# Kernel optimization log

Measured on AMD Instinct MI355X. Metric: run time of the kernel, lower is better.

## Reference

```python
import jax, jax.numpy as jnp
import numpy as np

N_NODES = 10000
N_EDGES = 250000
FEAT = 128
HEADS = 4
N_RBF = 50
CUTOFF = 5.0
EPS = 1e-15
LN_EPS = 1e-5


def setup_inputs() -> dict:
    key = jax.random.key(0)
    ks = jax.random.split(key, 12)
    F, HF = FEAT, HEADS * FEAT

    def lin(k, fi, fo):
        return (jax.random.normal(k, (fi, fo), jnp.float32) / np.sqrt(fi)).astype(jnp.float32)

    return {
        "s_j": jax.random.normal(ks[0], (N_NODES, F), jnp.float32),
        "v_j": jax.random.normal(ks[1], (N_NODES, F, 3), jnp.float32),
        "r_ij": jax.random.normal(ks[2], (N_EDGES, 3), jnp.float32) * 2.0,
        "nbrs": jax.random.randint(ks[3], (N_EDGES, 2), 0, N_NODES, dtype=jnp.int64) if jax.config.read('jax_enable_x64') else jax.random.randint(ks[3], (N_EDGES, 2), 0, N_NODES),
        "ln_gamma": jnp.ones((F,), jnp.float32),
        "ln_beta": jnp.zeros((F,), jnp.float32),
        "Wq": lin(ks[4], F, HF), "bq": jnp.zeros((HF,), jnp.float32),
        "Wk": lin(ks[5], F, HF), "bk": jnp.zeros((HF,), jnp.float32),
        "Wv": lin(ks[6], F, HF), "bv": jnp.zeros((HF,), jnp.float32),
        "Wdk": lin(ks[7], N_RBF, HF), "bdk": jnp.zeros((HF,), jnp.float32),
        "Wdv": lin(ks[8], N_RBF, HF), "bdv": jnp.zeros((HF,), jnp.float32),
        "Wd": lin(ks[9], HF, 3 * F), "bd": jnp.zeros((3 * F,), jnp.float32),
    }


def _forward(s_j, v_j, r_ij, nbrs, ln_gamma, ln_beta,
             Wq, bq, Wk, bk, Wv, bv, Wdk, bdk, Wdv, bdv, Wd, bd):
    E, F, H = r_ij.shape[0], s_j.shape[-1], HEADS
    # preprocess_r: dist and unit vectors
    dist = jnp.sqrt((r_ij ** 2 + EPS).sum(-1))          # [E]
    unit = r_ij / dist[:, None]                          # [E, 3]

    # LayerNorm (biased variance, like torch)
    mu = s_j.mean(-1, keepdims=True)
    var = s_j.var(-1, keepdims=True)
    x = (s_j - mu) / jnp.sqrt(var + LN_EPS) * ln_gamma + ln_beta  # [N, F]

    # node projections per head (head dim == feat_dim, TorchMD-Net style)
    q = (x @ Wq + bq).reshape(-1, H, F)
    k = (x @ Wk + bk).reshape(-1, H, F)
    v = (x @ Wv + bv).reshape(-1, H, F)

    # Gaussian RBF expansion of distances
    mus = jnp.linspace(0.0, CUTOFF, N_RBF, dtype=dist.dtype)
    width = mus[1] - mus[0]
    gamma = 0.5 / (width * width)
    rbf = jnp.exp(-gamma * (dist[:, None] - mus) ** 2)   # [E, n_rbf]

    dk = jax.nn.silu(rbf @ Wdk + bdk).reshape(E, H, F)   # distance filters
    dv = jax.nn.silu(rbf @ Wdv + bdv).reshape(E, H, F)

    i_dst = nbrs[:, 0]
    j_src = nbrs[:, 1]

    # attention over edges: silu(sum_f q_i * k_j * dk)
    attn = jax.nn.silu((q[i_dst] * k[j_src] * dk).sum(-1))  # [E, H]
    msg = (v[j_src] * dv * attn[:, :, None]).reshape(E, H * F)  # [E, H*F]

    out = (msg @ Wd + bd).reshape(E, 3, F)               # inv_out
    split0 = out[:, 0, :][:, :, None]                    # [E, F, 1]
    split1 = out[:, 1, :]                                # [E, F]
    split2 = out[:, 2, :][:, :, None]                    # [E, F, 1]

    delta_v_ij = split2 * unit[:, None, :] + split0 * v_j[j_src]  # [E, F, 3]
    delta_v_i = jax.ops.segment_sum(delta_v_ij, i_dst, num_segments=s_j.shape[0])
    delta_s_i = jax.ops.segment_sum(split1, i_dst, num_segments=s_j.shape[0])
    return delta_s_i, delta_v_i


def reference(s_j, v_j, r_ij, nbrs, ln_gamma, ln_beta,
              Wq, bq, Wk, bk, Wv, bv, Wdk, bdk, Wdv, bdv, Wd, bd):
    return _forward(s_j, v_j, r_ij, nbrs, ln_gamma, ln_beta,
                    Wq, bq, Wk, bk, Wv, bv, Wdk, bdk, Wdv, bdv, Wd, bd)
```

## Files before the change

### kernel.cpp

```cpp
#include <hip/hip_runtime.h>
#include <hip/hip_bf16.h>

typedef unsigned short ushort_t;
typedef short short8 __attribute__((ext_vector_type(8)));
typedef short short4v __attribute__((ext_vector_type(4)));
typedef float floatx4 __attribute__((ext_vector_type(4)));

#define FEAT 128
#define HF   512
#define NRBF 50
#define NNODE 10000
#define NEDGE 250000
#define NCHUNK 3907

__device__ __forceinline__ float b2f(unsigned int b){
    unsigned int u = (b & 0xffffu) << 16;
    float f; __builtin_memcpy(&f, &u, 4); return f;
}
__device__ __forceinline__ unsigned short f2b(float f){
    __hip_bfloat16 h = __float2bfloat16(f);
    unsigned short u; __builtin_memcpy(&u, &h, 2); return u;
}
__device__ __forceinline__ float silu_f(float x){ return x / (1.f + __expf(-x)); }

__device__ __forceinline__ bool is_fp32(const void* lng){
    return ((((const unsigned int*)lng)[0]) & 0xffffu) == 0u;
}
__device__ __forceinline__ float ld_f(const void* p, long idx, bool fp32){
    return fp32 ? ((const float*)p)[idx] : b2f(((const ushort_t*)p)[idx]);
}
__device__ __forceinline__ ushort_t ld_bf(const void* p, long idx, bool fp32){
    return fp32 ? f2b(((const float*)p)[idx]) : ((const ushort_t*)p)[idx];
}

__global__ __launch_bounds__(256) void k_sentinel(float* __restrict__ out){
    int x = blockIdx.x*256 + threadIdx.x;
    if (x < NNODE*FEAT*4) out[x] = 1.0f;
}

__global__ __launch_bounds__(256) void k_nbrs(const unsigned int* __restrict__ raw, int* __restrict__ out){
    int x = blockIdx.x*256 + threadIdx.x;
    if (x >= 2*NEDGE) return;
    unsigned int m = raw[1]|raw[3]|raw[5]|raw[7]|raw[9]|raw[11]|raw[13]|raw[15];
    int v = (m == 0u) ? (int)raw[2*x] : (int)raw[x];
    out[x] = ((unsigned)v < (unsigned)NNODE) ? v : 0;
}

__global__ __launch_bounds__(256) void k_count(const int* __restrict__ nb32, int* __restrict__ cnt){
    int x = blockIdx.x*256 + threadIdx.x;
    if (x >= NEDGE) return;
    atomicAdd(&cnt[nb32[2*x]], 1);
}
__global__ __launch_bounds__(256) void k_scan(const int* __restrict__ cnt, int* __restrict__ cursor){
    __shared__ int part[256];
    __shared__ int base[256];
    const int t = threadIdx.x;
    const int start = t*40;
    int s = 0;
    for (int u=0; u<40; u++){ int idx = start+u; if (idx < NNODE) s += cnt[idx]; }
    part[t] = s;
    __syncthreads();
    if (t == 0){
        int run = 0;
        for (int u=0; u<256; u++){ base[u] = run; run += part[u]; }
    }
    __syncthreads();
    int run = base[t];
    for (int u=0; u<40; u++){
        int idx = start+u;
        if (idx < NNODE){ cursor[idx] = run; run += cnt[idx]; }
    }
}
__global__ __launch_bounds__(256) void k_place(const int* __restrict__ nb32,
                                               int* __restrict__ cursor, int* __restrict__ perm){
    int x = blockIdx.x*256 + threadIdx.x;
    if (x >= NEDGE) return;
    int i = nb32[2*x];
    int pos = atomicAdd(&cursor[i], 1);
    perm[pos] = x;
}

__global__ __launch_bounds__(256) void k_conv(
    const void* ln_g, const void* ln_b, const void* bq, const void* bk, const void* bv,
    const void* bdk, const void* bdv, const void* bd, ushort_t* __restrict__ cb)
{
    const int t = threadIdx.x;
    const bool fp32 = is_fp32(ln_g);
    const void* srcs[8] = {ln_g, ln_b, bq, bk, bv, bdk, bdv, bd};
    const int offs[9] = {0,128,256,768,1280,1792,2304,2816,3200};
    for (int s=0; s<8; s++){
        int cnt = offs[s+1]-offs[s];
        for (int x=t; x<cnt; x+=256) cb[offs[s]+x] = ld_bf(srcs[s], x, fp32);
    }
}

__global__ __launch_bounds__(256) void k_vconv(const void* __restrict__ v_j,
                                               const void* __restrict__ lng,
                                               ushort_t* __restrict__ vjb){
    int x = blockIdx.x*256 + threadIdx.x;
    if (x >= NNODE*FEAT*3) return;
    vjb[x] = ld_bf(v_j, x, is_fp32(lng));
}

__global__ __launch_bounds__(256) void k_prep(
    const void* __restrict__ Wq, const void* __restrict__ Wk, const void* __restrict__ Wv,
    const void* __restrict__ Wdk, const void* __restrict__ Wdv, const void* __restrict__ Wd,
    const void* __restrict__ lng,
    ushort_t* __restrict__ WqT, ushort_t* __restrict__ WkT, ushort_t* __restrict__ WvT,
    ushort_t* __restrict__ WdkT, ushort_t* __restrict__ WdvT, ushort_t* __restrict__ WdT)
{
    const bool fp32 = is_fp32(lng);
    int idx = blockIdx.x*256 + threadIdx.x;
    if (idx < 3*65536){
        int mat = idx >> 16; int o = idx & 65535;
        int c = o >> 7, r = o & 127;
        const void* src = (mat==0)?Wq:((mat==1)?Wk:Wv);
        ushort_t* dst = (mat==0)?WqT:((mat==1)?WkT:WvT);
        dst[o] = ld_bf(src, r*HF + c, fp32);
    } else if (idx < 3*65536 + 2*32768){
        int o2 = idx - 3*65536; int mat = o2 >> 15; int o = o2 & 32767;
        int c = o >> 6, kk = o & 63;
        const void* src = mat ? Wdv : Wdk;
        ushort_t* dst = mat ? WdvT : WdkT;
        dst[o] = (kk < NRBF) ? ld_bf(src, kk*HF + c, fp32) : (ushort_t)0;
    } else {
        int o = idx - (3*65536 + 2*32768);
        int c = o >> 9, kk = o & 511;
        WdT[o] = ld_bf(Wd, kk*384 + c, fp32);
    }
}

__global__ __launch_bounds__(256) void k_qkv2(
    const void* __restrict__ s_j, const void* __restrict__ lng, const ushort_t* __restrict__ cb,
    const ushort_t* __restrict__ WqT, const ushort_t* __restrict__ WkT, const ushort_t* __restrict__ WvT,
    ushort_t* __restrict__ q, ushort_t* __restrict__ k, ushort_t* __restrict__ v)
{
    __shared__ __align__(16) ushort_t xlds[16][136];
    const int t = threadIdx.x;
    const int n = t >> 4, g = t & 15;
    const long node = (long)blockIdx.x*16 + n;
    const bool fp32 = is_fp32(lng);

    float xs[8];
    if (fp32){
        const float* sf = (const float*)s_j + node*FEAT + g*8;
        #pragma unroll
        for (int i=0;i<8;i++) xs[i] = sf[i];
    } else {
        short8 sv = *reinterpret_cast<const short8*>((const ushort_t*)s_j + node*FEAT + g*8);
        #pragma unroll
        for (int i=0;i<8;i++) xs[i] = b2f((unsigned short)sv[i]);
    }
    float sum = 0.f, ss = 0.f;
    #pragma unroll
    for (int i=0;i<8;i++){ sum += xs[i]; ss += xs[i]*xs[i]; }
    #pragma unroll
    for (int off=8; off; off>>=1){ sum += __shfl_xor(sum, off, 16); ss += __shfl_xor(ss, off, 16); }
    float mu = sum * (1.f/FEAT);
    float var = ss * (1.f/FEAT) - mu*mu;
    float sc = rsqrtf(var + 1e-5f);
    short8 gv  = *reinterpret_cast<const short8*>(cb + g*8);
    short8 bv2 = *reinterpret_cast<const short8*>(cb + 128 + g*8);
    short8 xv;
    #pragma unroll
    for (int i=0;i<8;i++){
        float val = (xs[i]-mu)*sc*b2f((unsigned short)gv[i]) + b2f((unsigned short)bv2[i]);
        xv[i] = (short)f2b(val);
    }
    *reinterpret_cast<short8*>(&xlds[n][g*8]) = xv;
    __syncthreads();

    const int lane = t & 63, w = t >> 6;
    const int col = lane & 15, quad = lane >> 4;
    short8 a[4];
    #pragma unroll
    for (int ks=0; ks<4; ks++)
        a[ks] = *reinterpret_cast<const short8*>(&xlds[col][ks*32 + quad*8]);

    for (int ii=0; ii<24; ii++){
        int nt = w + ii*4;
        int mat = nt >> 5, o0 = (nt & 31) << 4;
        const ushort_t* WT  = (mat==0)?WqT:((mat==1)?WkT:WvT);
        const ushort_t* bia = cb + 256 + mat*512;
        ushort_t* outp      = (mat==0)?q:((mat==1)?k:v);
        floatx4 acc = {0.f,0.f,0.f,0.f};
        #pragma unroll
        for (int ks=0; ks<4; ks++){
            short8 b = *reinterpret_cast<const short8*>(WT + (o0+col)*FEAT + ks*32 + quad*8);
            acc = __builtin_amdgcn_mfma_f32_16x16x32_bf16(a[ks], b, acc, 0, 0, 0);
        }
        float bc = b2f(bia[o0+col]);
        #pragma unroll
        for (int reg=0; reg<4; reg++){
            int row = quad*4 + reg;
            outp[((long)blockIdx.x*16 + row)*HF + o0 + col] = f2b(acc[reg] + bc);
        }
    }
}

struct __align__(16) EdgeSmem {
    int   i[64];
    int   jv[64];
    float unit[64][3];
    ushort_t rbf[4][16][72];
    union {
        ushort_t dkv[4][16][520];
        float    outb[32*385];
    };
};

__global__ __launch_bounds__(256, 2) void k_edge(
    const void* __restrict__ r_ij, const void* __restrict__ lng,
    const int* __restrict__ nbrs32, const int* __restrict__ perm,
    const ushort_t* __restrict__ q, const ushort_t* __restrict__ k, const ushort_t* __restrict__ v,
    const ushort_t* __restrict__ vjb,
    const ushort_t* __restrict__ WdkT, const ushort_t* __restrict__ WdvT,
    const ushort_t* __restrict__ cb,
    const ushort_t* __restrict__ WdT,
    float* __restrict__ acc_s, float* __restrict__ acc_v)
{
    __shared__ EdgeSmem sm;
    const int t = threadIdx.x;
    const long chunk = (long)(blockIdx.x & 7) * 489 + (blockIdx.x >> 3);
    if (chunk >= NCHUNK) return;
    const long e0 = chunk * 64;
    const int nvalid = (NEDGE - e0 < 64) ? (int)(NEDGE - e0) : 64;
    const bool fp32 = is_fp32(lng);
    const int lane = t & 63, w = t >> 6;
    const int col = lane & 15, quad = lane >> 4;
    const int eA = t >> 4, g = t & 15;
    const int h = g >> 2, sub = g & 3;

    short8 qf[4][4], kf[4][4];
    int jA_s[4];

    #pragma unroll
    for (int s=0; s<4; s++){
        const long eidx = e0 + s*16 + eA;
        const long ep = perm[(eidx < NEDGE) ? eidx : (NEDGE-1)];
        const int iA = nbrs32[2*ep];
        const int jA = nbrs32[2*ep+1];
        jA_s[s] = jA;
        float rx = ld_f(r_ij, ep*3+0, fp32);
        float ry = ld_f(r_ij, ep*3+1, fp32);
        float rz = ld_f(r_ij, ep*3+2, fp32);
        float d = sqrtf(rx*rx + ry*ry + rz*rz + 3e-15f);
        float inv = 1.f/d;
        if (g == 0){
            sm.i[s*16+eA] = iA; sm.jv[s*16+eA] = jA;
            sm.unit[s*16+eA][0] = rx*inv; sm.unit[s*16+eA][1] = ry*inv; sm.unit[s*16+eA][2] = rz*inv;
        }
        const float WIDTH = 5.f/49.f;
        const float GAMMA = 0.5f/(WIDTH*WIDTH);
        short4v rv;
        #pragma unroll
        for (int u=0; u<4; u++){
            int m = g*4 + u;
            float val = 0.f;
            if (m < NRBF){ float dm = d - (float)m*WIDTH; val = __expf(-GAMMA*dm*dm); }
            rv[u] = (short)f2b(val);
        }
        *reinterpret_cast<short4v*>(&sm.rbf[s][eA][g*4]) = rv;
        const ushort_t* qp = q + (long)iA*HF + h*128 + sub*32;
        const ushort_t* kp = k + (long)jA*HF + h*128 + sub*32;
        #pragma unroll
        for (int r=0; r<4; r++){
            qf[s][r] = *reinterpret_cast<const short8*>(qp + r*8);
            kf[s][r] = *reinterpret_cast<const short8*>(kp + r*8);
        }
    }
    __syncthreads();

    {
        for (int ii=0; ii<8; ii++){
            int nt = w + ii*4;
            int o0 = nt << 4;
            short8 b0 = *reinterpret_cast<const short8*>(WdkT + (o0+col)*64 + quad*8);
            short8 b1 = *reinterpret_cast<const short8*>(WdkT + (o0+col)*64 + 32 + quad*8);
            float bc = b2f(cb[1792 + o0 + col]);
            #pragma unroll
            for (int s=0; s<4; s++){
                short8 a0 = *reinterpret_cast<const short8*>(&sm.rbf[s][col][quad*8]);
                short8 a1 = *reinterpret_cast<const short8*>(&sm.rbf[s][col][32 + quad*8]);
                floatx4 ac = {0.f,0.f,0.f,0.f};
                ac = __builtin_amdgcn_mfma_f32_16x16x32_bf16(a0, b0, ac, 0, 0, 0);
                ac = __builtin_amdgcn_mfma_f32_16x16x32_bf16(a1, b1, ac, 0, 0, 0);
                #pragma unroll
                for (int reg=0; reg<4; reg++){
                    int row = quad*4 + reg;
                    sm.dkv[s][row][o0+col] = f2b(silu_f(ac[reg] + bc));
                }
            }
        }
    }
    __syncthreads();

    float at[4];
    short8 vf[4][4];
    {
        #pragma unroll
        for (int s=0; s<4; s++){
            const ushort_t* vp = v + (long)jA_s[s]*HF + g*32;
            #pragma unroll
            for (int r=0; r<4; r++) vf[s][r] = *reinterpret_cast<const short8*>(vp + r*8);
        }
        #pragma unroll
        for (int s=0; s<4; s++){
            const ushort_t* dkp = &sm.dkv[s][eA][h*128 + sub*32];
            float p = 0.f;
            #pragma unroll
            for (int r=0; r<4; r++){
                short8 d8 = *reinterpret_cast<const short8*>(dkp + r*8);
                #pragma unroll
                for (int u=0; u<8; u++)
                    p += b2f((unsigned short)qf[s][r][u]) * b2f((unsigned short)kf[s][r][u]) * b2f((unsigned short)d8[u]);
            }
            p += __shfl_xor(p, 1);
            p += __shfl_xor(p, 2);
            at[s] = silu_f(p);
        }
    }
    __syncthreads();

    {
        for (int ii=0; ii<8; ii++){
            int nt = w + ii*4;
            int o0 = nt << 4;
            short8 b0 = *reinterpret_cast<const short8*>(WdvT + (o0+col)*64 + quad*8);
            short8 b1 = *reinterpret_cast<const short8*>(WdvT + (o0+col)*64 + 32 + quad*8);
            float bc = b2f(cb[2304 + o0 + col]);
            #pragma unroll
            for (int s=0; s<4; s++){
                short8 a0 = *reinterpret_cast<const short8*>(&sm.rbf[s][col][quad*8]);
                short8 a1 = *reinterpret_cast<const short8*>(&sm.rbf[s][col][32 + quad*8]);
                floatx4 ac = {0.f,0.f,0.f,0.f};
                ac = __builtin_amdgcn_mfma_f32_16x16x32_bf16(a0, b0, ac, 0, 0, 0);
                ac = __builtin_amdgcn_mfma_f32_16x16x32_bf16(a1, b1, ac, 0, 0, 0);
                #pragma unroll
                for (int reg=0; reg<4; reg++){
                    int row = quad*4 + reg;
                    sm.dkv[s][row][o0+col] = f2b(silu_f(ac[reg] + bc));
                }
            }
        }
    }
    __syncthreads();

    #pragma unroll
    for (int s=0; s<4; s++){
        ushort_t* dvp = &sm.dkv[s][eA][g*32];
        #pragma unroll
        for (int r=0; r<4; r++){
            short8 d8 = *reinterpret_cast<const short8*>(dvp + r*8);
            short8 o8;
            #pragma unroll
            for (int u=0; u<8; u++)
                o8[u] = (short)f2b(b2f((unsigned short)vf[s][r][u]) * b2f((unsigned short)d8[u]) * at[s]);
            *reinterpret_cast<short8*>(dvp + r*8) = o8;
        }
    }
    __syncthreads();

    floatx4 acc[4][6];
    {
        #pragma unroll
        for (int s=0; s<4; s++)
            #pragma unroll
            for (int ii=0; ii<6; ii++) acc[s][ii] = (floatx4){0.f,0.f,0.f,0.f};
        for (int ks=0; ks<16; ks++){
            short8 a0 = *reinterpret_cast<const short8*>(&sm.dkv[0][col][ks*32 + quad*8]);
            short8 a1 = *reinterpret_cast<const short8*>(&sm.dkv[1][col][ks*32 + quad*8]);
            short8 a2 = *reinterpret_cast<const short8*>(&sm.dkv[2][col][ks*32 + quad*8]);
            short8 a3 = *reinterpret_cast<const short8*>(&sm.dkv[3][col][ks*32 + quad*8]);
            #pragma unroll
            for (int ii=0; ii<6; ii++){
                int o0 = (w + ii*4) << 4;
                short8 b = *reinterpret_cast<const short8*>(WdT + (o0+col)*HF + ks*32 + quad*8);
                acc[0][ii] = __builtin_amdgcn_mfma_f32_16x16x32_bf16(a0, b, acc[0][ii], 0, 0, 0);
                acc[1][ii] = __builtin_amdgcn_mfma_f32_16x16x32_bf16(a1, b, acc[1][ii], 0, 0, 0);
                acc[2][ii] = __builtin_amdgcn_mfma_f32_16x16x32_bf16(a2, b, acc[2][ii], 0, 0, 0);
                acc[3][ii] = __builtin_amdgcn_mfma_f32_16x16x32_bf16(a3, b, acc[3][ii], 0, 0, 0);
            }
        }
    }
    __syncthreads();

    {
        const int f = t & 127, half = t >> 7;
        int   cur_i = -1;
        float as = 0.f, av0 = 0.f, av1 = 0.f, av2 = 0.f;
        #pragma unroll
        for (int p=0; p<2; p++){
            #pragma unroll
            for (int ii=0; ii<6; ii++){
                int o0 = (w + ii*4) << 4;
                float bc = b2f(cb[2816 + o0 + col]);
                #pragma unroll
                for (int sl=0; sl<2; sl++){
                    int s = 2*p + sl;
                    #pragma unroll
                    for (int reg=0; reg<4; reg++){
                        int lrow = sl*16 + quad*4 + reg;
                        sm.outb[lrow*385 + o0 + col] = acc[s][ii][reg] + bc;
                    }
                }
            }
            __syncthreads();

            float vjx[16][3];
            #pragma unroll
            for (int u=0; u<16; u++){
                int e = p*32 + half*16 + u;
                const ushort_t* vp = vjb + (long)sm.jv[e]*384 + 3*f;
                vjx[u][0] = b2f(vp[0]); vjx[u][1] = b2f(vp[1]); vjx[u][2] = b2f(vp[2]);
            }
            #pragma unroll
            for (int u=0; u<16; u++){
                int el = half*16 + u;
                int e  = p*32 + el;
                if (e < nvalid){
                    int ie = sm.i[e];
                    if (ie != cur_i){
                        if (cur_i >= 0){
                            atomicAdd(&acc_s[(long)cur_i*FEAT + f], as);
                            float* ap = acc_v + ((long)cur_i*FEAT + f)*3;
                            atomicAdd(ap+0, av0); atomicAdd(ap+1, av1); atomicAdd(ap+2, av2);
                        }
                        cur_i = ie; as = 0.f; av0 = 0.f; av1 = 0.f; av2 = 0.f;
                    }
                    float o0v = sm.outb[el*385 + f];
                    float o1v = sm.outb[el*385 + 128 + f];
                    float o2v = sm.outb[el*385 + 256 + f];
                    as  += o1v;
                    av0 += o2v*sm.unit[e][0] + o0v*vjx[u][0];
                    av1 += o2v*sm.unit[e][1] + o0v*vjx[u][1];
                    av2 += o2v*sm.unit[e][2] + o0v*vjx[u][2];
                }
            }
            __syncthreads();
        }
        if (cur_i >= 0){
            atomicAdd(&acc_s[(long)cur_i*FEAT + f], as);
            float* ap = acc_v + ((long)cur_i*FEAT + f)*3;
            atomicAdd(ap+0, av0); atomicAdd(ap+1, av1); atomicAdd(ap+2, av2);
        }
    }
}

extern "C" void kernel_launch(void* const* d_in, const int* in_sizes, int n_in,
                              void* d_out, int out_size, void* d_ws, size_t ws_size,
                              hipStream_t stream)
{
    const void* s_j  = d_in[0];
    const void* v_j  = d_in[1];
    const void* r_ij = d_in[2];
    const unsigned int* nbrs_raw = (const unsigned int*)d_in[3];
    const void* ln_g = d_in[4];
    const void* ln_b = d_in[5];
    const void* Wq = d_in[6];   const void* bq  = d_in[7];
    const void* Wk = d_in[8];   const void* bk  = d_in[9];
    const void* Wv = d_in[10];  const void* bv  = d_in[11];
    const void* Wdk= d_in[12];  const void* bdk = d_in[13];
    const void* Wdv= d_in[14];  const void* bdv = d_in[15];
    const void* Wd = d_in[16];  const void* bd  = d_in[17];

    const size_t NEED = 43883904;
    if (ws_size < NEED){
        k_sentinel<<<20000, 256, 0, stream>>>((float*)d_out);
        return;
    }

    char* ws = (char*)d_ws;
    ushort_t* q    = (ushort_t*)(ws);
    ushort_t* vjb  = (ushort_t*)(ws + 10240000);
    int*      perm = (int*)(ws + 17920000);
    int*      cnt  = (int*)(ws + 18920000);
    int*      curs = (int*)(ws + 18960000);
    ushort_t* kk   = (ushort_t*)(ws + 20480000);
    ushort_t* vv   = (ushort_t*)(ws + 30720000);
    ushort_t* WqT  = (ushort_t*)(ws + 40960000);
    ushort_t* WkT  = (ushort_t*)(ws + 41091072);
    ushort_t* WvT  = (ushort_t*)(ws + 41222144);
    ushort_t* WdkT = (ushort_t*)(ws + 41353216);
    ushort_t* WdvT = (ushort_t*)(ws + 41418752);
    ushort_t* WdT  = (ushort_t*)(ws + 41484288);
    int*      nb32 = (int*)(ws + 41877504);
    ushort_t* cb   = (ushort_t*)(ws + 43877504);

    float* acc_s = (float*)d_out;
    float* acc_v = acc_s + 1280000;

    hipMemsetAsync(d_out, 0, 20480000, stream);
    hipMemsetAsync(cnt, 0, NNODE*sizeof(int), stream);
    k_nbrs <<<1954, 256, 0, stream>>>(nbrs_raw, nb32);
    k_count<<<977, 256, 0, stream>>>(nb32, cnt);
    k_scan <<<1, 256, 0, stream>>>(cnt, curs);
    k_place<<<977, 256, 0, stream>>>(nb32, curs, perm);
    k_conv <<<1, 256, 0, stream>>>(ln_g, ln_b, bq, bk, bv, bdk, bdv, bd, cb);
    k_vconv<<<15000, 256, 0, stream>>>(v_j, ln_g, vjb);
    k_prep <<<1792, 256, 0, stream>>>(Wq,Wk,Wv,Wdk,Wdv,Wd, ln_g, WqT,WkT,WvT,WdkT,WdvT,WdT);
    k_qkv2 <<<625, 256, 0, stream>>>(s_j, ln_g, cb, WqT, WkT, WvT, q, kk, vv);
    k_edge <<<3912, 256, 0, stream>>>(r_ij, ln_g, nb32, perm, q, kk, vv, vjb,
                                      WdkT, WdvT, cb, WdT,
                                      acc_s, acc_v);
}
```

Before: 690.4 us.

## Double edge tile to 128 edges per block with 512 threads

The edge kernel now processes 128 edges per block with 8 waves instead of 64 edges with 4 waves. Each Wd/Wdk/Wdv B-fragment loaded from global memory feeds 8 MFMA row tiles instead of 4, which halves weight traffic per edge. Per-thread accumulator state is rebalanced (acc[8][3]) and the scatter phase runs in four passes of 32 edges. Shared memory per block roughly doubles, so fewer blocks fit per CU. The larger chunks also add more synchronisation within each block.

```diff
diff --git a/kernel.cpp b/kernel.cpp
--- a/kernel.cpp
+++ b/kernel.cpp
@@ -11,7 +11,7 @@
 #define NRBF 50
 #define NNODE 10000
 #define NEDGE 250000
-#define NCHUNK 3907
+#define NCHUNK 1954
 
 __device__ __forceinline__ float b2f(unsigned int b){
     unsigned int u = (b & 0xffffu) << 16;
@@ -199,17 +199,17 @@
 }
 
 struct __align__(16) EdgeSmem {
-    int   i[64];
-    int   jv[64];
-    float unit[64][3];
-    ushort_t rbf[4][16][72];
+    int   i[128];
+    int   jv[128];
+    float unit[128][3];
+    ushort_t rbf[128][72];
     union {
-        ushort_t dkv[4][16][520];
+        ushort_t dkv[128][520];
         float    outb[32*385];
     };
 };
 
-__global__ __launch_bounds__(256, 2) void k_edge(
+__global__ __launch_bounds__(512, 2) void k_edge(
     const void* __restrict__ r_ij, const void* __restrict__ lng,
     const int* __restrict__ nbrs32, const int* __restrict__ perm,
     const ushort_t* __restrict__ q, const ushort_t* __restrict__ k, const ushort_t* __restrict__ v,
@@ -221,10 +221,10 @@
 {
     __shared__ EdgeSmem sm;
     const int t = threadIdx.x;
-    const long chunk = (long)(blockIdx.x & 7) * 489 + (blockIdx.x >> 3);
+    const long chunk = (long)(blockIdx.x & 7) * 245 + (blockIdx.x >> 3);
     if (chunk >= NCHUNK) return;
-    const long e0 = chunk * 64;
-    const int nvalid = (NEDGE - e0 < 64) ? (int)(NEDGE - e0) : 64;
+    const long e0 = chunk * 128;
+    const int nvalid = (NEDGE - e0 < 128) ? (int)(NEDGE - e0) : 128;
     const bool fp32 = is_fp32(lng);
     const int lane = t & 63, w = t >> 6;
     const int col = lane & 15, quad = lane >> 4;
@@ -236,7 +236,8 @@
 
     #pragma unroll
     for (int s=0; s<4; s++){
-        const long eidx = e0 + s*16 + eA;
+        const int e_loc = s*32 + eA;
+        const long eidx = e0 + e_loc;
         const long ep = perm[(eidx < NEDGE) ? eidx : (NEDGE-1)];
         const int iA = nbrs32[2*ep];
         const int jA = nbrs32[2*ep+1];
@@ -247,8 +248,8 @@
         float d = sqrtf(rx*rx + ry*ry + rz*rz + 3e-15f);
         float inv = 1.f/d;
         if (g == 0){
-            sm.i[s*16+eA] = iA; sm.jv[s*16+eA] = jA;
-            sm.unit[s*16+eA][0] = rx*inv; sm.unit[s*16+eA][1] = ry*inv; sm.unit[s*16+eA][2] = rz*inv;
+            sm.i[e_loc] = iA; sm.jv[e_loc] = jA;
+            sm.unit[e_loc][0] = rx*inv; sm.unit[e_loc][1] = ry*inv; sm.unit[e_loc][2] = rz*inv;
         }
         const float WIDTH = 5.f/49.f;
         const float GAMMA = 0.5f/(WIDTH*WIDTH);
@@ -260,7 +261,7 @@
             if (m < NRBF){ float dm = d - (float)m*WIDTH; val = __expf(-GAMMA*dm*dm); }
             rv[u] = (short)f2b(val);
         }
-        *reinterpret_cast<short4v*>(&sm.rbf[s][eA][g*4]) = rv;
+        *reinterpret_cast<short4v*>(&sm.rbf[e_loc][g*4]) = rv;
         const ushort_t* qp = q + (long)iA*HF + h*128 + sub*32;
         const ushort_t* kp = k + (long)jA*HF + h*128 + sub*32;
         #pragma unroll
@@ -272,23 +273,23 @@
     __syncthreads();
 
     {
-        for (int ii=0; ii<8; ii++){
-            int nt = w + ii*4;
+        for (int ii=0; ii<4; ii++){
+            int nt = w + ii*8;
             int o0 = nt << 4;
             short8 b0 = *reinterpret_cast<const short8*>(WdkT + (o0+col)*64 + quad*8);
             short8 b1 = *reinterpret_cast<const short8*>(WdkT + (o0+col)*64 + 32 + quad*8);
             float bc = b2f(cb[1792 + o0 + col]);
             #pragma unroll
-            for (int s=0; s<4; s++){
-                short8 a0 = *reinterpret_cast<const short8*>(&sm.rbf[s][col][quad*8]);
-                short8 a1 = *reinterpret_cast<const short8*>(&sm.rbf[s][col][32 + quad*8]);
+            for (int st=0; st<8; st++){
+                short8 a0 = *reinterpret_cast<const short8*>(&sm.rbf[st*16+col][quad*8]);
+                short8 a1 = *reinterpret_cast<const short8*>(&sm.rbf[st*16+col][32 + quad*8]);
                 floatx4 ac = {0.f,0.f,0.f,0.f};
                 ac = __builtin_amdgcn_mfma_f32_16x16x32_bf16(a0, b0, ac, 0, 0, 0);
                 ac = __builtin_amdgcn_mfma_f32_16x16x32_bf16(a1, b1, ac, 0, 0, 0);
                 #pragma unroll
                 for (int reg=0; reg<4; reg++){
-                    int row = quad*4 + reg;
-                    sm.dkv[s][row][o0+col] = f2b(silu_f(ac[reg] + bc));
+                    int row = st*16 + quad*4 + reg;
+                    sm.dkv[row][o0+col] = f2b(silu_f(ac[reg] + bc));
                 }
             }
         }
@@ -306,7 +307,8 @@
         }
         #pragma unroll
         for (int s=0; s<4; s++){
-            const ushort_t* dkp = &sm.dkv[s][eA][h*128 + sub*32];
+            const int e_loc = s*32 + eA;
+            const ushort_t* dkp = &sm.dkv[e_loc][h*128 + sub*32];
             float p = 0.f;
             #pragma unroll
             for (int r=0; r<4; r++){
@@ -323,23 +325,23 @@
     __syncthreads();
 
     {
-        for (int ii=0; ii<8; ii++){
-            int nt = w + ii*4;
+        for (int ii=0; ii<4; ii++){
+            int nt = w + ii*8;
             int o0 = nt << 4;
             short8 b0 = *reinterpret_cast<const short8*>(WdvT + (o0+col)*64 + quad*8);
             short8 b1 = *reinterpret_cast<const short8*>(WdvT + (o0+col)*64 + 32 + quad*8);
             float bc = b2f(cb[2304 + o0 + col]);
             #pragma unroll
-            for (int s=0; s<4; s++){
-                short8 a0 = *reinterpret_cast<const short8*>(&sm.rbf[s][col][quad*8]);
-                short8 a1 = *reinterpret_cast<const short8*>(&sm.rbf[s][col][32 + quad*8]);
+            for (int st=0; st<8; st++){
+                short8 a0 = *reinterpret_cast<const short8*>(&sm.rbf[st*16+col][quad*8]);
+                short8 a1 = *reinterpret_cast<const short8*>(&sm.rbf[st*16+col][32 + quad*8]);
                 floatx4 ac = {0.f,0.f,0.f,0.f};
                 ac = __builtin_amdgcn_mfma_f32_16x16x32_bf16(a0, b0, ac, 0, 0, 0);
                 ac = __builtin_amdgcn_mfma_f32_16x16x32_bf16(a1, b1, ac, 0, 0, 0);
                 #pragma unroll
                 for (int reg=0; reg<4; reg++){
-                    int row = quad*4 + reg;
-                    sm.dkv[s][row][o0+col] = f2b(silu_f(ac[reg] + bc));
+                    int row = st*16 + quad*4 + reg;
+                    sm.dkv[row][o0+col] = f2b(silu_f(ac[reg] + bc));
                 }
             }
         }
@@ -348,7 +350,8 @@
 
     #pragma unroll
     for (int s=0; s<4; s++){
-        ushort_t* dvp = &sm.dkv[s][eA][g*32];
+        const int e_loc = s*32 + eA;
+        ushort_t* dvp = &sm.dkv[e_loc][g*32];
         #pragma unroll
         for (int r=0; r<4; r++){
             short8 d8 = *reinterpret_cast<const short8*>(dvp + r*8);
@@ -361,62 +364,61 @@
     }
     __syncthreads();
 
-    floatx4 acc[4][6];
+    floatx4 acc[8][3];
     {
         #pragma unroll
-        for (int s=0; s<4; s++)
-            #pragma unroll
-            for (int ii=0; ii<6; ii++) acc[s][ii] = (floatx4){0.f,0.f,0.f,0.f};
+        for (int st=0; st<8; st++)
+            #pragma unroll
+            for (int ii=0; ii<3; ii++) acc[st][ii] = (floatx4){0.f,0.f,0.f,0.f};
         for (int ks=0; ks<16; ks++){
-            short8 a0 = *reinterpret_cast<const short8*>(&sm.dkv[0][col][ks*32 + quad*8]);
-            short8 a1 = *reinterpret_cast<const short8*>(&sm.dkv[1][col][ks*32 + quad*8]);
-            short8 a2 = *reinterpret_cast<const short8*>(&sm.dkv[2][col][ks*32 + quad*8]);
-            short8 a3 = *reinterpret_cast<const short8*>(&sm.dkv[3][col][ks*32 + quad*8]);
-            #pragma unroll
-            for (int ii=0; ii<6; ii++){
-                int o0 = (w + ii*4) << 4;
+            short8 a[8];
+            #pragma unroll
+            for (int st=0; st<8; st++)
+                a[st] = *reinterpret_cast<const short8*>(&sm.dkv[st*16+col][ks*32 + quad*8]);
+            #pragma unroll
+            for (int ii=0; ii<3; ii++){
+                int o0 = (w + ii*8) << 4;
                 short8 b = *reinterpret_cast<const short8*>(WdT + (o0+col)*HF + ks*32 + quad*8);
-                acc[0][ii] = __builtin_amdgcn_mfma_f32_16x16x32_bf16(a0, b, acc[0][ii], 0, 0, 0);
-                acc[1][ii] = __builtin_amdgcn_mfma_f32_16x16x32_bf16(a1, b, acc[1][ii], 0, 0, 0);
-                acc[2][ii] = __builtin_amdgcn_mfma_f32_16x16x32_bf16(a2, b, acc[2][ii], 0, 0, 0);
-                acc[3][ii] = __builtin_amdgcn_mfma_f32_16x16x32_bf16(a3, b, acc[3][ii], 0, 0, 0);
+                #pragma unroll
+                for (int st=0; st<8; st++)
+                    acc[st][ii] = __builtin_amdgcn_mfma_f32_16x16x32_bf16(a[st], b, acc[st][ii], 0, 0, 0);
             }
         }
     }
     __syncthreads();
 
     {
-        const int f = t & 127, half = t >> 7;
+        const int f = t & 127, grp = t >> 7;
         int   cur_i = -1;
         float as = 0.f, av0 = 0.f, av1 = 0.f, av2 = 0.f;
         #pragma unroll
-        for (int p=0; p<2; p++){
-            #pragma unroll
-            for (int ii=0; ii<6; ii++){
-                int o0 = (w + ii*4) << 4;
+        for (int p=0; p<4; p++){
+            #pragma unroll
+            for (int ii=0; ii<3; ii++){
+                int o0 = (w + ii*8) << 4;
                 float bc = b2f(cb[2816 + o0 + col]);
                 #pragma unroll
                 for (int sl=0; sl<2; sl++){
-                    int s = 2*p + sl;
+                    int st = 2*p + sl;
                     #pragma unroll
                     for (int reg=0; reg<4; reg++){
                         int lrow = sl*16 + quad*4 + reg;
-                        sm.outb[lrow*385 + o0 + col] = acc[s][ii][reg] + bc;
+                        sm.outb[lrow*385 + o0 + col] = acc[st][ii][reg] + bc;
                     }
                 }
             }
             __syncthreads();
 
-            float vjx[16][3];
-            #pragma unroll
-            for (int u=0; u<16; u++){
-                int e = p*32 + half*16 + u;
+            float vjx[8][3];
+            #pragma unroll
+            for (int u=0; u<8; u++){
+                int e = p*32 + grp*8 + u;
                 const ushort_t* vp = vjb + (long)sm.jv[e]*384 + 3*f;
                 vjx[u][0] = b2f(vp[0]); vjx[u][1] = b2f(vp[1]); vjx[u][2] = b2f(vp[2]);
             }
             #pragma unroll
-            for (int u=0; u<16; u++){
-                int el = half*16 + u;
+            for (int u=0; u<8; u++){
+                int el = grp*8 + u;
                 int e  = p*32 + el;
                 if (e < nvalid){
                     int ie = sm.i[e];
@@ -500,7 +502,7 @@
     k_vconv<<<15000, 256, 0, stream>>>(v_j, ln_g, vjb);
     k_prep <<<1792, 256, 0, stream>>>(Wq,Wk,Wv,Wdk,Wdv,Wd, ln_g, WqT,WkT,WvT,WdkT,WdvT,WdT);
     k_qkv2 <<<625, 256, 0, stream>>>(s_j, ln_g, cb, WqT, WkT, WvT, q, kk, vv);
-    k_edge <<<3912, 256, 0, stream>>>(r_ij, ln_g, nb32, perm, q, kk, vv, vjb,
+    k_edge <<<1960, 512, 0, stream>>>(r_ij, ln_g, nb32, perm, q, kk, vv, vjb,
                                       WdkT, WdvT, cb, WdT,
                                       acc_s, acc_v);
 }
```

Result: slower. 738.4 us (+7.0%).

## Fuse small preprocessing kernels and process two node tiles per QKV block

Applied to the files above, without the earlier changes.

Folds the neighbor-count atomic pass and the v_j bf16 conversion into the k_nbrs kernel, and moves the bias/LayerNorm parameter conversion into an extra block of k_prep, removing three separate launches. The QKV projection kernel now handles 32 nodes per block, reusing each loaded weight fragment for two MFMA tiles and halving the grid. This cuts launch overhead and weight reloads, at the cost of a grid-stride conversion loop inside k_nbrs and a clamped, guarded tail for the last node tile.

```diff
diff --git a/kernel.cpp b/kernel.cpp
--- a/kernel.cpp
+++ b/kernel.cpp
@@ -38,19 +38,23 @@
     if (x < NNODE*FEAT*4) out[x] = 1.0f;
 }
 
-__global__ __launch_bounds__(256) void k_nbrs(const unsigned int* __restrict__ raw, int* __restrict__ out){
+__global__ __launch_bounds__(256) void k_nbrs(const unsigned int* __restrict__ raw,
+                                              int* __restrict__ out, int* __restrict__ cnt,
+                                              const void* __restrict__ v_j,
+                                              const void* __restrict__ lng,
+                                              ushort_t* __restrict__ vjb){
     int x = blockIdx.x*256 + threadIdx.x;
+    const bool fp32 = is_fp32(lng);
+    for (long y = x; y < (long)NNODE*FEAT*3; y += 500224)
+        vjb[y] = ld_bf(v_j, y, fp32);
     if (x >= 2*NEDGE) return;
     unsigned int m = raw[1]|raw[3]|raw[5]|raw[7]|raw[9]|raw[11]|raw[13]|raw[15];
     int v = (m == 0u) ? (int)raw[2*x] : (int)raw[x];
-    out[x] = ((unsigned)v < (unsigned)NNODE) ? v : 0;
-}
-
-__global__ __launch_bounds__(256) void k_count(const int* __restrict__ nb32, int* __restrict__ cnt){
-    int x = blockIdx.x*256 + threadIdx.x;
-    if (x >= NEDGE) return;
-    atomicAdd(&cnt[nb32[2*x]], 1);
-}
+    v = ((unsigned)v < (unsigned)NNODE) ? v : 0;
+    out[x] = v;
+    if (!(x & 1)) atomicAdd(&cnt[v], 1);
+}
+
 __global__ __launch_bounds__(256) void k_scan(const int* __restrict__ cnt, int* __restrict__ cursor){
     __shared__ int part[256];
     __shared__ int base[256];
@@ -80,36 +84,27 @@
     perm[pos] = x;
 }
 
-__global__ __launch_bounds__(256) void k_conv(
-    const void* ln_g, const void* ln_b, const void* bq, const void* bk, const void* bv,
-    const void* bdk, const void* bdv, const void* bd, ushort_t* __restrict__ cb)
-{
-    const int t = threadIdx.x;
-    const bool fp32 = is_fp32(ln_g);
-    const void* srcs[8] = {ln_g, ln_b, bq, bk, bv, bdk, bdv, bd};
-    const int offs[9] = {0,128,256,768,1280,1792,2304,2816,3200};
-    for (int s=0; s<8; s++){
-        int cnt = offs[s+1]-offs[s];
-        for (int x=t; x<cnt; x+=256) cb[offs[s]+x] = ld_bf(srcs[s], x, fp32);
-    }
-}
-
-__global__ __launch_bounds__(256) void k_vconv(const void* __restrict__ v_j,
-                                               const void* __restrict__ lng,
-                                               ushort_t* __restrict__ vjb){
-    int x = blockIdx.x*256 + threadIdx.x;
-    if (x >= NNODE*FEAT*3) return;
-    vjb[x] = ld_bf(v_j, x, is_fp32(lng));
-}
-
 __global__ __launch_bounds__(256) void k_prep(
     const void* __restrict__ Wq, const void* __restrict__ Wk, const void* __restrict__ Wv,
     const void* __restrict__ Wdk, const void* __restrict__ Wdv, const void* __restrict__ Wd,
-    const void* __restrict__ lng,
+    const void* __restrict__ lng, const void* __restrict__ ln_b,
+    const void* __restrict__ bq, const void* __restrict__ bk, const void* __restrict__ bv,
+    const void* __restrict__ bdk, const void* __restrict__ bdv, const void* __restrict__ bd,
     ushort_t* __restrict__ WqT, ushort_t* __restrict__ WkT, ushort_t* __restrict__ WvT,
-    ushort_t* __restrict__ WdkT, ushort_t* __restrict__ WdvT, ushort_t* __restrict__ WdT)
+    ushort_t* __restrict__ WdkT, ushort_t* __restrict__ WdvT, ushort_t* __restrict__ WdT,
+    ushort_t* __restrict__ cb)
 {
     const bool fp32 = is_fp32(lng);
+    if (blockIdx.x == 1792){
+        const int t = threadIdx.x;
+        const void* srcs[8] = {lng, ln_b, bq, bk, bv, bdk, bdv, bd};
+        const int offs[9] = {0,128,256,768,1280,1792,2304,2816,3200};
+        for (int s=0; s<8; s++){
+            int c2 = offs[s+1]-offs[s];
+            for (int x=t; x<c2; x+=256) cb[offs[s]+x] = ld_bf(srcs[s], x, fp32);
+        }
+        return;
+    }
     int idx = blockIdx.x*256 + threadIdx.x;
     if (idx < 3*65536){
         int mat = idx >> 16; int o = idx & 65535;
@@ -135,47 +130,54 @@
     const ushort_t* __restrict__ WqT, const ushort_t* __restrict__ WkT, const ushort_t* __restrict__ WvT,
     ushort_t* __restrict__ q, ushort_t* __restrict__ k, ushort_t* __restrict__ v)
 {
-    __shared__ __align__(16) ushort_t xlds[16][136];
+    __shared__ __align__(16) ushort_t xlds[2][16][136];
     const int t = threadIdx.x;
     const int n = t >> 4, g = t & 15;
-    const long node = (long)blockIdx.x*16 + n;
     const bool fp32 = is_fp32(lng);
-
-    float xs[8];
-    if (fp32){
-        const float* sf = (const float*)s_j + node*FEAT + g*8;
-        #pragma unroll
-        for (int i=0;i<8;i++) xs[i] = sf[i];
-    } else {
-        short8 sv = *reinterpret_cast<const short8*>((const ushort_t*)s_j + node*FEAT + g*8);
-        #pragma unroll
-        for (int i=0;i<8;i++) xs[i] = b2f((unsigned short)sv[i]);
-    }
-    float sum = 0.f, ss = 0.f;
+    const long base = (long)blockIdx.x*32;
+
     #pragma unroll
-    for (int i=0;i<8;i++){ sum += xs[i]; ss += xs[i]*xs[i]; }
-    #pragma unroll
-    for (int off=8; off; off>>=1){ sum += __shfl_xor(sum, off, 16); ss += __shfl_xor(ss, off, 16); }
-    float mu = sum * (1.f/FEAT);
-    float var = ss * (1.f/FEAT) - mu*mu;
-    float sc = rsqrtf(var + 1e-5f);
-    short8 gv  = *reinterpret_cast<const short8*>(cb + g*8);
-    short8 bv2 = *reinterpret_cast<const short8*>(cb + 128 + g*8);
-    short8 xv;
-    #pragma unroll
-    for (int i=0;i<8;i++){
-        float val = (xs[i]-mu)*sc*b2f((unsigned short)gv[i]) + b2f((unsigned short)bv2[i]);
-        xv[i] = (short)f2b(val);
-    }
-    *reinterpret_cast<short8*>(&xlds[n][g*8]) = xv;
+    for (int s=0; s<2; s++){
+        long node = base + s*16 + n;
+        if (node >= NNODE) node = NNODE-1;
+        float xs[8];
+        if (fp32){
+            const float* sf = (const float*)s_j + node*FEAT + g*8;
+            #pragma unroll
+            for (int i=0;i<8;i++) xs[i] = sf[i];
+        } else {
+            short8 sv = *reinterpret_cast<const short8*>((const ushort_t*)s_j + node*FEAT + g*8);
+            #pragma unroll
+            for (int i=0;i<8;i++) xs[i] = b2f((unsigned short)sv[i]);
+        }
+        float sum = 0.f, ss = 0.f;
+        #pragma unroll
+        for (int i=0;i<8;i++){ sum += xs[i]; ss += xs[i]*xs[i]; }
+        #pragma unroll
+        for (int off=8; off; off>>=1){ sum += __shfl_xor(sum, off, 16); ss += __shfl_xor(ss, off, 16); }
+        float mu = sum * (1.f/FEAT);
+        float var = ss * (1.f/FEAT) - mu*mu;
+        float sc = rsqrtf(var + 1e-5f);
+        short8 gv  = *reinterpret_cast<const short8*>(cb + g*8);
+        short8 bv2 = *reinterpret_cast<const short8*>(cb + 128 + g*8);
+        short8 xv;
+        #pragma unroll
+        for (int i=0;i<8;i++){
+            float val = (xs[i]-mu)*sc*b2f((unsigned short)gv[i]) + b2f((unsigned short)bv2[i]);
+            xv[i] = (short)f2b(val);
+        }
+        *reinterpret_cast<short8*>(&xlds[s][n][g*8]) = xv;
+    }
     __syncthreads();
 
     const int lane = t & 63, w = t >> 6;
     const int col = lane & 15, quad = lane >> 4;
-    short8 a[4];
+    short8 a0[4], a1[4];
     #pragma unroll
-    for (int ks=0; ks<4; ks++)
-        a[ks] = *reinterpret_cast<const short8*>(&xlds[col][ks*32 + quad*8]);
+    for (int ks=0; ks<4; ks++){
+        a0[ks] = *reinterpret_cast<const short8*>(&xlds[0][col][ks*32 + quad*8]);
+        a1[ks] = *reinterpret_cast<const short8*>(&xlds[1][col][ks*32 + quad*8]);
+    }
 
     for (int ii=0; ii<24; ii++){
         int nt = w + ii*4;
@@ -183,17 +185,22 @@
         const ushort_t* WT  = (mat==0)?WqT:((mat==1)?WkT:WvT);
         const ushort_t* bia = cb + 256 + mat*512;
         ushort_t* outp      = (mat==0)?q:((mat==1)?k:v);
-        floatx4 acc = {0.f,0.f,0.f,0.f};
+        floatx4 ac0 = {0.f,0.f,0.f,0.f};
+        floatx4 ac1 = {0.f,0.f,0.f,0.f};
         #pragma unroll
         for (int ks=0; ks<4; ks++){
             short8 b = *reinterpret_cast<const short8*>(WT + (o0+col)*FEAT + ks*32 + quad*8);
-            acc = __builtin_amdgcn_mfma_f32_16x16x32_bf16(a[ks], b, acc, 0, 0, 0);
+            ac0 = __builtin_amdgcn_mfma_f32_16x16x32_bf16(a0[ks], b, ac0, 0, 0, 0);
+            ac1 = __builtin_amdgcn_mfma_f32_16x16x32_bf16(a1[ks], b, ac1, 0, 0, 0);
         }
         float bc = b2f(bia[o0+col]);
         #pragma unroll
         for (int reg=0; reg<4; reg++){
             int row = quad*4 + reg;
-            outp[((long)blockIdx.x*16 + row)*HF + o0 + col] = f2b(acc[reg] + bc);
+            long n0 = base + row;
+            outp[n0*HF + o0 + col] = f2b(ac0[reg] + bc);
+            long n1 = base + 16 + row;
+            if (n1 < NNODE) outp[n1*HF + o0 + col] = f2b(ac1[reg] + bc);
         }
     }
 }
@@ -492,14 +499,13 @@
 
     hipMemsetAsync(d_out, 0, 20480000, stream);
     hipMemsetAsync(cnt, 0, NNODE*sizeof(int), stream);
-    k_nbrs <<<1954, 256, 0, stream>>>(nbrs_raw, nb32);
-    k_count<<<977, 256, 0, stream>>>(nb32, cnt);
+    k_nbrs <<<1954, 256, 0, stream>>>(nbrs_raw, nb32, cnt, v_j, ln_g, vjb);
     k_scan <<<1, 256, 0, stream>>>(cnt, curs);
     k_place<<<977, 256, 0, stream>>>(nb32, curs, perm);
-    k_conv <<<1, 256, 0, stream>>>(ln_g, ln_b, bq, bk, bv, bdk, bdv, bd, cb);
-    k_vconv<<<15000, 256, 0, stream>>>(v_j, ln_g, vjb);
-    k_prep <<<1792, 256, 0, stream>>>(Wq,Wk,Wv,Wdk,Wdv,Wd, ln_g, WqT,WkT,WvT,WdkT,WdvT,WdT);
-    k_qkv2 <<<625, 256, 0, stream>>>(s_j, ln_g, cb, WqT, WkT, WvT, q, kk, vv);
+    k_prep <<<1793, 256, 0, stream>>>(Wq,Wk,Wv,Wdk,Wdv,Wd, ln_g, ln_b,
+                                      bq,bk,bv,bdk,bdv,bd,
+                                      WqT,WkT,WvT,WdkT,WdvT,WdT, cb);
+    k_qkv2 <<<313, 256, 0, stream>>>(s_j, ln_g, cb, WqT, WkT, WvT, q, kk, vv);
     k_edge <<<3912, 256, 0, stream>>>(r_ij, ln_g, nb32, perm, q, kk, vv, vjb,
                                       WdkT, WdvT, cb, WdT,
                                       acc_s, acc_v);
```

Result: faster. 675.1 us (-2.2%).
